# Kernel tuning notes

Measured on AMD Instinct MI355X. Metric: run time of the kernel, lower is better.

## Reference

```python
import jax, jax.numpy as jnp
import numpy as np
from jax import lax

POOL = 2  # pool_kernel

def _conv2d(x, w, b, stride=1):
    # x: [N,C,H,W], w: [O,I,kh,kw] (torch OIHW layout)
    y = lax.conv_general_dilated(
        x, w, window_strides=(stride, stride), padding='VALID',
        dimension_numbers=('NCHW', 'OIHW', 'NCHW'))
    return y + b[None, :, None, None]

def _maxpool(x, k):
    return lax.reduce_window(x, -jnp.inf, lax.max,
                             (1, 1, k, k), (1, 1, k, k), 'VALID')

def setup_inputs() -> dict:
    key = jax.random.key(0)
    ks = jax.random.split(key, 8)
    B, S, D = 8, 64, 128
    C = 32  # num_channels, depth=3 -> channels 1->32->64->64
    def kaiming(k, shape):
        fan_in = shape[1] * shape[2] * shape[3]
        return jax.random.normal(k, shape, jnp.float32) * np.float32(np.sqrt(2.0 / fan_in))
    return {
        'token_features': jax.random.normal(ks[0], (B, S, D), jnp.float32),
        'type_embedds': jax.random.normal(ks[1], (B, S, D), jnp.float32),
        'w0': kaiming(ks[2], (C, 1, 3, 3)),
        'b0': jnp.zeros((C,), jnp.float32),
        'w1': kaiming(ks[3], (2 * C, C, 3, 3)),
        'b1': jnp.zeros((2 * C,), jnp.float32),
        'w2': kaiming(ks[4], (2 * C, 2 * C, 3, 3)),
        'b2': jnp.zeros((2 * C,), jnp.float32),
    }

def reference(token_features, type_embedds, w0, b0, w1, b1, w2, b2):
    B, S, D = type_embedds.shape
    # Outter2dFusion: ger(gate, features) -> fused[b,s,i,j] = type[b,s,i]*token[b,s,j]
    fused = jnp.einsum('bsi,bsj->bsij', type_embedds, token_features)
    x = fused.reshape(B * S, 1, D, D)  # each token's d x d map as 1-channel image
    gelu = lambda t: jax.nn.gelu(t, approximate=False)  # torch GELU default (erf)
    x = _maxpool(gelu(_conv2d(x, w0, b0, stride=1)), POOL)
    x = _maxpool(gelu(_conv2d(x, w1, b1, stride=1)), POOL)
    x = _maxpool(gelu(_conv2d(x, w2, b2, stride=1)), POOL)
    # dropout is identity at inference
    return x.reshape(B, S, -1)
```

## Files before the change

### kernel.cpp

```cpp
#include <hip/hip_runtime.h>


typedef short short8 __attribute__((ext_vector_type(8)));
typedef _Float16 half8 __attribute__((ext_vector_type(8)));
typedef float f32x4 __attribute__((ext_vector_type(4)));
typedef unsigned int uint4v __attribute__((ext_vector_type(4)));

#define OFF_TY   0
#define OFF_H16  544
#define OFF_P0   32800
#define OFF_P1   100384
#define OFF_TK   OFF_P0
#define LDS_TOTAL 123936

__device__ __forceinline__ unsigned short f2bf(float f) {
    unsigned int u = __float_as_uint(f);
    u += 0x7fffu + ((u >> 16) & 1u);
    return (unsigned short)(u >> 16);
}

__device__ __forceinline__ unsigned int pack2h(float a, float b) {
    union { _Float16 h[2]; unsigned int u; } p;
    p.h[0] = (_Float16)a;
    p.h[1] = (_Float16)b;
    return p.u;
}

__device__ __forceinline__ float gelu_f(float x) {
    float ax = __builtin_fabsf(x);
    float E  = __builtin_amdgcn_exp2f(x * x * -0.72134752f);
    float k  = __builtin_amdgcn_rcpf(__builtin_fmaf(0.33267686f, ax, 1.0f));
    float s  = __builtin_fmaf(0.7478556f, k, -0.0958798f);
    s = __builtin_fmaf(s, k, 0.3480242f);
    s = s * k;
    float erfabs = __builtin_fmaf(-s, E, 1.0f);
    return __builtin_fmaf(0.5f * ax, erfabs, 0.5f * x);
}

__device__ __forceinline__ void conv0_burst(char* smem, const float* tys,
                                            int w, int l15, int lc,
                                            float b00, float b01, int pbase) {
    const int y_base = 2 * pbase;
    half8 afrag;
    {
        float a0 = tys[y_base + l15 + 0];
        float a1 = tys[y_base + l15 + 1];
        float a2 = tys[y_base + l15 + 2];
        float a3 = tys[y_base + l15 + 3];
        union { uint4v u; half8 h; } av;
        av.u = (uint4v){ pack2h(a0, a1), pack2h(a2, a3), 0u, 0u };
        afrag = av.h;
    }
    const f32x4 ci0 = (f32x4){b00, b00, b00, b00};
    const f32x4 ci1 = (f32x4){b01, b01, b01, b01};
    const int base = (w < 4) ? w * 12 : 48 + (w - 4) * 20;
    const int cnt  = (w < 4) ? 12 : ((w == 7) ? 18 : 20);

    #pragma unroll
    for (int j = 0; j < 20; ++j) {
        if (j < cnt) {
            const int uid = base + j;
            const int q  = uid >> 1;
            const int ct = uid & 1;
            const char* hp = smem + OFF_H16 + ((2*q)*32 + ct*16 + l15) * 8;
            uint2 hA = *(const uint2*)(hp);
            uint2 hB = *(const uint2*)(hp + 256);
            if (lc != 0) { hA.x = 0u; hA.y = 0u; hB.x = 0u; hB.y = 0u; }
            union { uint4v u; half8 h; } ba, bb;
            ba.u = (uint4v){hA.x, hA.y, 0u, 0u};
            bb.u = (uint4v){hB.x, hB.y, 0u, 0u};
            const f32x4 ci = ct ? ci1 : ci0;
            f32x4 cA = __builtin_amdgcn_mfma_f32_16x16x32_f16(afrag, ba.h, ci, 0, 0, 0);
            f32x4 cB = __builtin_amdgcn_mfma_f32_16x16x32_f16(afrag, bb.h, ci, 0, 0, 0);
            float m0 = gelu_f(fmaxf(fmaxf(cA[0], cA[1]), fmaxf(cB[0], cB[1])));
            float m1 = gelu_f(fmaxf(fmaxf(cA[2], cA[3]), fmaxf(cB[2], cB[3])));
            const int c = ct * 16 + l15;
            const int upos = (q >> 1) * 8 + ((4 * (q & 1) + (c >> 3)) ^ ((q >> 1) & 7));
            const int p0 = pbase + 2 * lc;
            const int s0 = p0 & 15, s1 = (p0 + 1) & 15;
            *(unsigned short*)(smem + OFF_P0 + (s0 * 264 + upos) * 16 + (c & 7) * 2) = f2bf(m0);
            *(unsigned short*)(smem + OFF_P0 + (s1 * 264 + upos) * 16 + (c & 7) * 2) = f2bf(m1);
        }
    }
}

__launch_bounds__(512, 2)
__global__ void conv_pipeline(const float* __restrict__ token,
                              const float* __restrict__ type_,
                              const float* __restrict__ w0, const float* __restrict__ b0,
                              const float* __restrict__ w1, const float* __restrict__ b1,
                              const float* __restrict__ w2, const float* __restrict__ b2,
                              float* __restrict__ out) {
    extern __shared__ char smem[];
    float* tys = (float*)(smem + OFF_TY);
    float* tks = (float*)(smem + OFF_TK);

    const int tid = threadIdx.x;
    const int img = blockIdx.x;
    const int w   = tid >> 6;
    const int l   = tid & 63;
    const int l15 = l & 15;
    const int lc  = l >> 4;
    const int c0w = tid & 31;

    for (int i = tid; i < 132; i += 512) {
        tys[i] = (i < 128) ? type_[img*128 + i] : 0.f;
        if (i < 128) tks[i] = token[img*128 + i];
    }

    const float b00 = b0[l15];
    const float b01 = b0[l15 + 16];

    __syncthreads();

    {
        float w0r[9];
        #pragma unroll
        for (int i = 0; i < 9; ++i) w0r[i] = w0[c0w*9 + i];
        int x = tid >> 5;
        #pragma unroll
        for (int k = 0; k < 8; ++k, x += 16) {
            if (x < 126) {
                float t0 = tks[x], t1 = tks[x+1], t2 = tks[x+2];
                float h0 = __builtin_fmaf(w0r[0],t0, __builtin_fmaf(w0r[1],t1, w0r[2]*t2));
                float h1 = __builtin_fmaf(w0r[3],t0, __builtin_fmaf(w0r[4],t1, w0r[5]*t2));
                float h2 = __builtin_fmaf(w0r[6],t0, __builtin_fmaf(w0r[7],t1, w0r[8]*t2));
                uint2 hv; hv.x = pack2h(h0, h1); hv.y = pack2h(h2, 0.f);
                *(uint2*)(smem + OFF_H16 + (x*32 + c0w)*8) = hv;
            }
        }
    }

    short8 wf[18];
    float bias;
    const int ch = ((w & 3) * 16) + l15;
    if (w < 4) {
        bias = b1[ch];
        #pragma unroll
        for (int uv = 0; uv < 9; ++uv) {
            short8 f;
            #pragma unroll
            for (int j = 0; j < 8; ++j)
                f[j] = (short)f2bf(w1[(ch*32 + 8*lc + j)*9 + uv]);
            wf[uv] = f;
        }
    } else {
        bias = b2[ch];
        #pragma unroll
        for (int kh = 0; kh < 2; ++kh)
            #pragma unroll
            for (int uv = 0; uv < 9; ++uv) {
                short8 f;
                #pragma unroll
                for (int j = 0; j < 8; ++j)
                    f[j] = (short)f2bf(w2[(ch*64 + kh*32 + 8*lc + j)*9 + uv]);
                wf[kh*9 + uv] = f;
            }
    }

    __syncthreads();

    conv0_burst(smem, tys, w, l15, lc, b00, b01, 0);
    __syncthreads();

    const size_t obase = (size_t)img * 12544;

    for (int i1 = 0; i1 < 30; ++i1) {
        if (w < 4) {
            int rbase = (i1 % 6) * 30;
            int xr = ch >> 3;
            #pragma unroll
            for (int half = 0; half < 2; ++half) {
                f32x4 acc[4];
                #pragma unroll
                for (int i = 0; i < 4; ++i) acc[i] = (f32x4){0.f,0.f,0.f,0.f};
                #pragma unroll
                for (int pr = 0; pr < 4; ++pr) {
                    int sbase = ((2*i1 + pr) & 15) * 264;
                    #pragma unroll
                    for (int v = 0; v < 3; ++v) {
                        #pragma unroll
                        for (int mtl = 0; mtl < 2; ++mtl) {
                            int col = (2*half + mtl)*16 + l15 + v;
                            int unit = sbase + (col>>1)*8 + ((4*(col&1) + lc) ^ ((col>>1)&7));
                            short8 a = *(const short8*)(smem + OFF_P0 + unit*16);
                            if (pr <= 2)
                                acc[mtl*2+0] = __builtin_amdgcn_mfma_f32_16x16x32_bf16(
                                    a, wf[pr*3+v], acc[mtl*2+0], 0, 0, 0);
                            if (pr >= 1)
                                acc[mtl*2+1] = __builtin_amdgcn_mfma_f32_16x16x32_bf16(
                                    a, wf[(pr-1)*3+v], acc[mtl*2+1], 0, 0, 0);
                        }
                    }
                }
                #pragma unroll
                for (int mtl = 0; mtl < 2; ++mtl) {
                    int pcol = (2*half + mtl)*8 + lc*2;
                    if (pcol < 30) {
                        f32x4 A0 = acc[mtl*2+0], A1 = acc[mtl*2+1];
                        float p0 = fmaxf(fmaxf(A0[0], A0[1]), fmaxf(A1[0], A1[1]));
                        float p1 = fmaxf(fmaxf(A0[2], A0[3]), fmaxf(A1[2], A1[3]));
                        float m0 = gelu_f(p0 + bias);
                        float m1 = gelu_f(p1 + bias);
                        int u0 = (rbase + pcol)*8     + (xr ^ (pcol & 7));
                        int u1 = (rbase + pcol + 1)*8 + (xr ^ ((pcol+1) & 7));
                        *(unsigned short*)(smem + OFF_P1 + u0*16 + (ch&7)*2) = f2bf(m0);
                        *(unsigned short*)(smem + OFF_P1 + u1*16 + (ch&7)*2) = f2bf(m1);
                    }
                }
            }
        } else if (i1 >= 4 && (i1 & 1) == 0) {
            const int i2 = (i1 - 4) >> 1;
            f32x4 acc[4];
            #pragma unroll
            for (int i = 0; i < 4; ++i) acc[i] = (f32x4){0.f,0.f,0.f,0.f};
            #pragma unroll
            for (int pr = 0; pr < 4; ++pr) {
                int rb = ((2*i2 + pr) % 6) * 30;
                #pragma unroll
                for (int v = 0; v < 3; ++v) {
                    #pragma unroll
                    for (int mt = 0; mt < 2; ++mt) {
                        int col = mt*16 + l15 + v;
                        #pragma unroll
                        for (int kh = 0; kh < 2; ++kh) {
                            int unit = (rb + col)*8 + ((kh*4 + lc) ^ (col & 7));
                            short8 a = *(const short8*)(smem + OFF_P1 + unit*16);
                            if (pr <= 2)
                                acc[mt*2+0] = __builtin_amdgcn_mfma_f32_16x16x32_bf16(
                                    a, wf[kh*9 + pr*3+v], acc[mt*2+0], 0, 0, 0);
                            if (pr >= 1)
                                acc[mt*2+1] = __builtin_amdgcn_mfma_f32_16x16x32_bf16(
                                    a, wf[kh*9 + (pr-1)*3+v], acc[mt*2+1], 0, 0, 0);
                        }
                    }
                }
            }
            #pragma unroll
            for (int mt = 0; mt < 2; ++mt) {
                int pcol = mt*8 + lc*2;
                if (pcol < 14) {
                    f32x4 A0 = acc[mt*2+0], A1 = acc[mt*2+1];
                    float g00 = gelu_f(A0[0] + bias), g01 = gelu_f(A0[1] + bias);
                    float g02 = gelu_f(A0[2] + bias), g03 = gelu_f(A0[3] + bias);
                    float g10 = gelu_f(A1[0] + bias), g11 = gelu_f(A1[1] + bias);
                    float g12 = gelu_f(A1[2] + bias), g13 = gelu_f(A1[3] + bias);
                    float m0 = fmaxf(fmaxf(g00, g01), fmaxf(g10, g11));
                    float m1 = fmaxf(fmaxf(g02, g03), fmaxf(g12, g13));
                    float2 st; st.x = m0; st.y = m1;
                    *(float2*)(out + obase + ch*196 + i2*14 + pcol) = st;
                }
            }
        }

        if ((i1 & 3) == 2) conv0_burst(smem, tys, w, l15, lc, b00, b01, 2*i1 + 4);

        __syncthreads();
    }

    if (w >= 4) {
        const int i2 = 13;
        f32x4 acc[4];
        #pragma unroll
        for (int i = 0; i < 4; ++i) acc[i] = (f32x4){0.f,0.f,0.f,0.f};
        #pragma unroll
        for (int pr = 0; pr < 4; ++pr) {
            int rb = ((2*i2 + pr) % 6) * 30;
            #pragma unroll
            for (int v = 0; v < 3; ++v) {
                #pragma unroll
                for (int mt = 0; mt < 2; ++mt) {
                    int col = mt*16 + l15 + v;
                    #pragma unroll
                    for (int kh = 0; kh < 2; ++kh) {
                        int unit = (rb + col)*8 + ((kh*4 + lc) ^ (col & 7));
                        short8 a = *(const short8*)(smem + OFF_P1 + unit*16);
                        if (pr <= 2)
                            acc[mt*2+0] = __builtin_amdgcn_mfma_f32_16x16x32_bf16(
                                a, wf[kh*9 + pr*3+v], acc[mt*2+0], 0, 0, 0);
                        if (pr >= 1)
                            acc[mt*2+1] = __builtin_amdgcn_mfma_f32_16x16x32_bf16(
                                a, wf[kh*9 + (pr-1)*3+v], acc[mt*2+1], 0, 0, 0);
                    }
                }
            }
        }
        #pragma unroll
        for (int mt = 0; mt < 2; ++mt) {
            int pcol = mt*8 + lc*2;
            if (pcol < 14) {
                f32x4 A0 = acc[mt*2+0], A1 = acc[mt*2+1];
                float g00 = gelu_f(A0[0] + bias), g01 = gelu_f(A0[1] + bias);
                float g02 = gelu_f(A0[2] + bias), g03 = gelu_f(A0[3] + bias);
                float g10 = gelu_f(A1[0] + bias), g11 = gelu_f(A1[1] + bias);
                float g12 = gelu_f(A1[2] + bias), g13 = gelu_f(A1[3] + bias);
                float m0 = fmaxf(fmaxf(g00, g01), fmaxf(g10, g11));
                float m1 = fmaxf(fmaxf(g02, g03), fmaxf(g12, g13));
                float2 st; st.x = m0; st.y = m1;
                *(float2*)(out + obase + ch*196 + i2*14 + pcol) = st;
            }
        }
    }
}

extern "C" void kernel_launch(void* const* d_in, const int* in_sizes, int n_in,
                              void* d_out, int out_size, void* d_ws, size_t ws_size,
                              hipStream_t stream) {
    const float* token = (const float*)d_in[0];
    const float* type_ = (const float*)d_in[1];
    const float* w0 = (const float*)d_in[2];
    const float* b0 = (const float*)d_in[3];
    const float* w1 = (const float*)d_in[4];
    const float* b1 = (const float*)d_in[5];
    const float* w2 = (const float*)d_in[6];
    const float* b2 = (const float*)d_in[7];
    float* out = (float*)d_out;

    hipLaunchKernelGGL(conv_pipeline, dim3(512), dim3(512), LDS_TOTAL, stream,
                       token, type_, w0, b0, w1, b1, w2, b2, out);
}
```

Measured before the change: 187.3 us.

## Double block size to 1024 threads and split conv work across 16 waves

Raises the workgroup from 8 to 16 waves. Conv1 waves each take one half of the columns instead of looping over both halves, conv2 waves each take one M-tile, and the conv0 burst units are redistributed across 16 waves. This gives more waves per image to hide MFMA and LDS latency, at the cost of a lower occupancy bound (one block per CU) and tighter register limits under the 1024-thread launch bound.

After: 251.4 us. +34.2%, slower.

```diff
diff --git a/kernel.cpp b/kernel.cpp
--- a/kernel.cpp
+++ b/kernel.cpp
@@ -53,11 +53,11 @@
     }
     const f32x4 ci0 = (f32x4){b00, b00, b00, b00};
     const f32x4 ci1 = (f32x4){b01, b01, b01, b01};
-    const int base = (w < 4) ? w * 12 : 48 + (w - 4) * 20;
-    const int cnt  = (w < 4) ? 12 : ((w == 7) ? 18 : 20);
+    const int base = (w < 8) ? w * 6 : 48 + (w - 8) * 10;
+    const int cnt  = (w < 8) ? 6 : ((w == 15) ? 8 : 10);
 
     #pragma unroll
-    for (int j = 0; j < 20; ++j) {
+    for (int j = 0; j < 10; ++j) {
         if (j < cnt) {
             const int uid = base + j;
             const int q  = uid >> 1;
@@ -84,7 +84,7 @@
     }
 }
 
-__launch_bounds__(512, 2)
+__launch_bounds__(1024, 1)
 __global__ void conv_pipeline(const float* __restrict__ token,
                               const float* __restrict__ type_,
                               const float* __restrict__ w0, const float* __restrict__ b0,
@@ -103,7 +103,7 @@
     const int lc  = l >> 4;
     const int c0w = tid & 31;
 
-    for (int i = tid; i < 132; i += 512) {
+    for (int i = tid; i < 132; i += 1024) {
         tys[i] = (i < 128) ? type_[img*128 + i] : 0.f;
         if (i < 128) tks[i] = token[img*128 + i];
     }
@@ -119,7 +119,7 @@
         for (int i = 0; i < 9; ++i) w0r[i] = w0[c0w*9 + i];
         int x = tid >> 5;
         #pragma unroll
-        for (int k = 0; k < 8; ++k, x += 16) {
+        for (int k = 0; k < 4; ++k, x += 32) {
             if (x < 126) {
                 float t0 = tks[x], t1 = tks[x+1], t2 = tks[x+2];
                 float h0 = __builtin_fmaf(w0r[0],t0, __builtin_fmaf(w0r[1],t1, w0r[2]*t2));
@@ -134,7 +134,7 @@
     short8 wf[18];
     float bias;
     const int ch = ((w & 3) * 16) + l15;
-    if (w < 4) {
+    if (w < 8) {
         bias = b1[ch];
         #pragma unroll
         for (int uv = 0; uv < 9; ++uv) {
@@ -166,139 +166,123 @@
     const size_t obase = (size_t)img * 12544;
 
     for (int i1 = 0; i1 < 30; ++i1) {
-        if (w < 4) {
+        if (w < 8) {
+            const int half = w >> 2;
             int rbase = (i1 % 6) * 30;
             int xr = ch >> 3;
-            #pragma unroll
-            for (int half = 0; half < 2; ++half) {
-                f32x4 acc[4];
+            f32x4 acc[4];
+            #pragma unroll
+            for (int i = 0; i < 4; ++i) acc[i] = (f32x4){0.f,0.f,0.f,0.f};
+            #pragma unroll
+            for (int pr = 0; pr < 4; ++pr) {
+                int sbase = ((2*i1 + pr) & 15) * 264;
                 #pragma unroll
-                for (int i = 0; i < 4; ++i) acc[i] = (f32x4){0.f,0.f,0.f,0.f};
-                #pragma unroll
-                for (int pr = 0; pr < 4; ++pr) {
-                    int sbase = ((2*i1 + pr) & 15) * 264;
+                for (int v = 0; v < 3; ++v) {
                     #pragma unroll
-                    for (int v = 0; v < 3; ++v) {
-                        #pragma unroll
-                        for (int mtl = 0; mtl < 2; ++mtl) {
-                            int col = (2*half + mtl)*16 + l15 + v;
-                            int unit = sbase + (col>>1)*8 + ((4*(col&1) + lc) ^ ((col>>1)&7));
-                            short8 a = *(const short8*)(smem + OFF_P0 + unit*16);
-                            if (pr <= 2)
-                                acc[mtl*2+0] = __builtin_amdgcn_mfma_f32_16x16x32_bf16(
-                                    a, wf[pr*3+v], acc[mtl*2+0], 0, 0, 0);
-                            if (pr >= 1)
-                                acc[mtl*2+1] = __builtin_amdgcn_mfma_f32_16x16x32_bf16(
-                                    a, wf[(pr-1)*3+v], acc[mtl*2+1], 0, 0, 0);
-                        }
+                    for (int mtl = 0; mtl < 2; ++mtl) {
+                        int col = (2*half + mtl)*16 + l15 + v;
+                        int unit = sbase + (col>>1)*8 + ((4*(col&1) + lc) ^ ((col>>1)&7));
+                        short8 a = *(const short8*)(smem + OFF_P0 + unit*16);
+                        if (pr <= 2)
+                            acc[mtl*2+0] = __builtin_amdgcn_mfma_f32_16x16x32_bf16(
+                                a, wf[pr*3+v], acc[mtl*2+0], 0, 0, 0);
+                        if (pr >= 1)
+                            acc[mtl*2+1] = __builtin_amdgcn_mfma_f32_16x16x32_bf16(
+                                a, wf[(pr-1)*3+v], acc[mtl*2+1], 0, 0, 0);
                     }
                 }
-                #pragma unroll
-                for (int mtl = 0; mtl < 2; ++mtl) {
-                    int pcol = (2*half + mtl)*8 + lc*2;
-                    if (pcol < 30) {
-                        f32x4 A0 = acc[mtl*2+0], A1 = acc[mtl*2+1];
-                        float p0 = fmaxf(fmaxf(A0[0], A0[1]), fmaxf(A1[0], A1[1]));
-                        float p1 = fmaxf(fmaxf(A0[2], A0[3]), fmaxf(A1[2], A1[3]));
-                        float m0 = gelu_f(p0 + bias);
-                        float m1 = gelu_f(p1 + bias);
-                        int u0 = (rbase + pcol)*8     + (xr ^ (pcol & 7));
-                        int u1 = (rbase + pcol + 1)*8 + (xr ^ ((pcol+1) & 7));
-                        *(unsigned short*)(smem + OFF_P1 + u0*16 + (ch&7)*2) = f2bf(m0);
-                        *(unsigned short*)(smem + OFF_P1 + u1*16 + (ch&7)*2) = f2bf(m1);
-                    }
+            }
+            #pragma unroll
+            for (int mtl = 0; mtl < 2; ++mtl) {
+                int pcol = (2*half + mtl)*8 + lc*2;
+                if (pcol < 30) {
+                    f32x4 A0 = acc[mtl*2+0], A1 = acc[mtl*2+1];
+                    float p0 = fmaxf(fmaxf(A0[0], A0[1]), fmaxf(A1[0], A1[1]));
+                    float p1 = fmaxf(fmaxf(A0[2], A0[3]), fmaxf(A1[2], A1[3]));
+                    float m0 = gelu_f(p0 + bias);
+                    float m1 = gelu_f(p1 + bias);
+                    int u0 = (rbase + pcol)*8     + (xr ^ (pcol & 7));
+                    int u1 = (rbase + pcol + 1)*8 + (xr ^ ((pcol+1) & 7));
+                    *(unsigned short*)(smem + OFF_P1 + u0*16 + (ch&7)*2) = f2bf(m0);
+                    *(unsigned short*)(smem + OFF_P1 + u1*16 + (ch&7)*2) = f2bf(m1);
                 }
             }
         } else if (i1 >= 4 && (i1 & 1) == 0) {
             const int i2 = (i1 - 4) >> 1;
-            f32x4 acc[4];
-            #pragma unroll
-            for (int i = 0; i < 4; ++i) acc[i] = (f32x4){0.f,0.f,0.f,0.f};
+            const int mt = (w >> 2) & 1;
+            f32x4 acc0 = (f32x4){0.f,0.f,0.f,0.f};
+            f32x4 acc1 = (f32x4){0.f,0.f,0.f,0.f};
             #pragma unroll
             for (int pr = 0; pr < 4; ++pr) {
                 int rb = ((2*i2 + pr) % 6) * 30;
                 #pragma unroll
                 for (int v = 0; v < 3; ++v) {
-                    #pragma unroll
-                    for (int mt = 0; mt < 2; ++mt) {
-                        int col = mt*16 + l15 + v;
-                        #pragma unroll
-                        for (int kh = 0; kh < 2; ++kh) {
-                            int unit = (rb + col)*8 + ((kh*4 + lc) ^ (col & 7));
-                            short8 a = *(const short8*)(smem + OFF_P1 + unit*16);
-                            if (pr <= 2)
-                                acc[mt*2+0] = __builtin_amdgcn_mfma_f32_16x16x32_bf16(
-                                    a, wf[kh*9 + pr*3+v], acc[mt*2+0], 0, 0, 0);
-                            if (pr >= 1)
-                                acc[mt*2+1] = __builtin_amdgcn_mfma_f32_16x16x32_bf16(
-                                    a, wf[kh*9 + (pr-1)*3+v], acc[mt*2+1], 0, 0, 0);
-                        }
-                    }
-                }
-            }
-            #pragma unroll
-            for (int mt = 0; mt < 2; ++mt) {
-                int pcol = mt*8 + lc*2;
-                if (pcol < 14) {
-                    f32x4 A0 = acc[mt*2+0], A1 = acc[mt*2+1];
-                    float g00 = gelu_f(A0[0] + bias), g01 = gelu_f(A0[1] + bias);
-                    float g02 = gelu_f(A0[2] + bias), g03 = gelu_f(A0[3] + bias);
-                    float g10 = gelu_f(A1[0] + bias), g11 = gelu_f(A1[1] + bias);
-                    float g12 = gelu_f(A1[2] + bias), g13 = gelu_f(A1[3] + bias);
-                    float m0 = fmaxf(fmaxf(g00, g01), fmaxf(g10, g11));
-                    float m1 = fmaxf(fmaxf(g02, g03), fmaxf(g12, g13));
-                    float2 st; st.x = m0; st.y = m1;
-                    *(float2*)(out + obase + ch*196 + i2*14 + pcol) = st;
-                }
-            }
-        }
-
-        if ((i1 & 3) == 2) conv0_burst(smem, tys, w, l15, lc, b00, b01, 2*i1 + 4);
-
-        __syncthreads();
-    }
-
-    if (w >= 4) {
-        const int i2 = 13;
-        f32x4 acc[4];
-        #pragma unroll
-        for (int i = 0; i < 4; ++i) acc[i] = (f32x4){0.f,0.f,0.f,0.f};
-        #pragma unroll
-        for (int pr = 0; pr < 4; ++pr) {
-            int rb = ((2*i2 + pr) % 6) * 30;
-            #pragma unroll
-            for (int v = 0; v < 3; ++v) {
-                #pragma unroll
-                for (int mt = 0; mt < 2; ++mt) {
                     int col = mt*16 + l15 + v;
                     #pragma unroll
                     for (int kh = 0; kh < 2; ++kh) {
                         int unit = (rb + col)*8 + ((kh*4 + lc) ^ (col & 7));
                         short8 a = *(const short8*)(smem + OFF_P1 + unit*16);
                         if (pr <= 2)
-                            acc[mt*2+0] = __builtin_amdgcn_mfma_f32_16x16x32_bf16(
-                                a, wf[kh*9 + pr*3+v], acc[mt*2+0], 0, 0, 0);
+                            acc0 = __builtin_amdgcn_mfma_f32_16x16x32_bf16(
+                                a, wf[kh*9 + pr*3+v], acc0, 0, 0, 0);
                         if (pr >= 1)
-                            acc[mt*2+1] = __builtin_amdgcn_mfma_f32_16x16x32_bf16(
-                                a, wf[kh*9 + (pr-1)*3+v], acc[mt*2+1], 0, 0, 0);
+                            acc1 = __builtin_amdgcn_mfma_f32_16x16x32_bf16(
+                                a, wf[kh*9 + (pr-1)*3+v], acc1, 0, 0, 0);
                     }
                 }
             }
-        }
-        #pragma unroll
-        for (int mt = 0; mt < 2; ++mt) {
             int pcol = mt*8 + lc*2;
             if (pcol < 14) {
-                f32x4 A0 = acc[mt*2+0], A1 = acc[mt*2+1];
-                float g00 = gelu_f(A0[0] + bias), g01 = gelu_f(A0[1] + bias);
-                float g02 = gelu_f(A0[2] + bias), g03 = gelu_f(A0[3] + bias);
-                float g10 = gelu_f(A1[0] + bias), g11 = gelu_f(A1[1] + bias);
-                float g12 = gelu_f(A1[2] + bias), g13 = gelu_f(A1[3] + bias);
+                float g00 = gelu_f(acc0[0] + bias), g01 = gelu_f(acc0[1] + bias);
+                float g02 = gelu_f(acc0[2] + bias), g03 = gelu_f(acc0[3] + bias);
+                float g10 = gelu_f(acc1[0] + bias), g11 = gelu_f(acc1[1] + bias);
+                float g12 = gelu_f(acc1[2] + bias), g13 = gelu_f(acc1[3] + bias);
                 float m0 = fmaxf(fmaxf(g00, g01), fmaxf(g10, g11));
                 float m1 = fmaxf(fmaxf(g02, g03), fmaxf(g12, g13));
                 float2 st; st.x = m0; st.y = m1;
                 *(float2*)(out + obase + ch*196 + i2*14 + pcol) = st;
             }
+        }
+
+        if ((i1 & 3) == 2) conv0_burst(smem, tys, w, l15, lc, b00, b01, 2*i1 + 4);
+
+        __syncthreads();
+    }
+
+    if (w >= 8) {
+        const int i2 = 13;
+        const int mt = (w >> 2) & 1;
+        f32x4 acc0 = (f32x4){0.f,0.f,0.f,0.f};
+        f32x4 acc1 = (f32x4){0.f,0.f,0.f,0.f};
+        #pragma unroll
+        for (int pr = 0; pr < 4; ++pr) {
+            int rb = ((2*i2 + pr) % 6) * 30;
+            #pragma unroll
+            for (int v = 0; v < 3; ++v) {
+                int col = mt*16 + l15 + v;
+                #pragma unroll
+                for (int kh = 0; kh < 2; ++kh) {
+                    int unit = (rb + col)*8 + ((kh*4 + lc) ^ (col & 7));
+                    short8 a = *(const short8*)(smem + OFF_P1 + unit*16);
+                    if (pr <= 2)
+                        acc0 = __builtin_amdgcn_mfma_f32_16x16x32_bf16(
+                            a, wf[kh*9 + pr*3+v], acc0, 0, 0, 0);
+                    if (pr >= 1)
+                        acc1 = __builtin_amdgcn_mfma_f32_16x16x32_bf16(
+                            a, wf[kh*9 + (pr-1)*3+v], acc1, 0, 0, 0);
+                }
+            }
+        }
+        int pcol = mt*8 + lc*2;
+        if (pcol < 14) {
+            float g00 = gelu_f(acc0[0] + bias), g01 = gelu_f(acc0[1] + bias);
+            float g02 = gelu_f(acc0[2] + bias), g03 = gelu_f(acc0[3] + bias);
+            float g10 = gelu_f(acc1[0] + bias), g11 = gelu_f(acc1[1] + bias);
+            float g12 = gelu_f(acc1[2] + bias), g13 = gelu_f(acc1[3] + bias);
+            float m0 = fmaxf(fmaxf(g00, g01), fmaxf(g10, g11));
+            float m1 = fmaxf(fmaxf(g02, g03), fmaxf(g12, g13));
+            float2 st; st.x = m0; st.y = m1;
+            *(float2*)(out + obase + ch*196 + i2*14 + pcol) = st;
         }
     }
 }
@@ -316,6 +300,6 @@
     const float* b2 = (const float*)d_in[7];
     float* out = (float*)d_out;
 
-    hipLaunchKernelGGL(conv_pipeline, dim3(512), dim3(512), LDS_TOTAL, stream,
+    hipLaunchKernelGGL(conv_pipeline, dim3(512), dim3(1024), LDS_TOTAL, stream,
                        token, type_, w0, b0, w1, b1, w2, b2, out);
 }
```

## Split conv2 over two iterations, halve barriers, and raise MFMA wave priority

Applied to the files above, without the earlier changes.

Splits each conv2 output row's accumulation across two consecutive loop iterations, keeping the accumulators live in registers between them. This balances conv2 work against conv1 work every iteration instead of every other one. It also moves the conv0 burst earlier, issues __syncthreads only on odd iterations, and wraps the MFMA sections in s_setprio. The aim is to cut idle time for the conv2 waves and barrier overhead, at the cost of more register pressure and tighter ring-buffer hazard margins.

Result: slower. 462.9 us, median of 2 (+147.1%).

```diff
diff --git a/kernel.cpp b/kernel.cpp
--- a/kernel.cpp
+++ b/kernel.cpp
@@ -165,10 +165,13 @@
 
     const size_t obase = (size_t)img * 12544;
 
+    f32x4 c2acc[4];
+
     for (int i1 = 0; i1 < 30; ++i1) {
         if (w < 4) {
             int rbase = (i1 % 6) * 30;
             int xr = ch >> 3;
+            __builtin_amdgcn_s_setprio(1);
             #pragma unroll
             for (int half = 0; half < 2; ++half) {
                 f32x4 acc[4];
@@ -193,6 +196,7 @@
                         }
                     }
                 }
+                __builtin_amdgcn_s_setprio(0);
                 #pragma unroll
                 for (int mtl = 0; mtl < 2; ++mtl) {
                     int pcol = (2*half + mtl)*8 + lc*2;
@@ -208,14 +212,19 @@
                         *(unsigned short*)(smem + OFF_P1 + u1*16 + (ch&7)*2) = f2bf(m1);
                     }
                 }
-            }
-        } else if (i1 >= 4 && (i1 & 1) == 0) {
+                if (half == 0) __builtin_amdgcn_s_setprio(1);
+            }
+        } else if (i1 >= 4) {
             const int i2 = (i1 - 4) >> 1;
-            f32x4 acc[4];
-            #pragma unroll
-            for (int i = 0; i < 4; ++i) acc[i] = (f32x4){0.f,0.f,0.f,0.f};
-            #pragma unroll
-            for (int pr = 0; pr < 4; ++pr) {
+            const int prlo = (i1 & 1) ? 2 : 0;
+            if ((i1 & 1) == 0) {
+                #pragma unroll
+                for (int i = 0; i < 4; ++i) c2acc[i] = (f32x4){0.f,0.f,0.f,0.f};
+            }
+            __builtin_amdgcn_s_setprio(1);
+            #pragma unroll
+            for (int prr = 0; prr < 2; ++prr) {
+                const int pr = prlo + prr;
                 int rb = ((2*i2 + pr) % 6) * 30;
                 #pragma unroll
                 for (int v = 0; v < 3; ++v) {
@@ -227,35 +236,39 @@
                             int unit = (rb + col)*8 + ((kh*4 + lc) ^ (col & 7));
                             short8 a = *(const short8*)(smem + OFF_P1 + unit*16);
                             if (pr <= 2)
-                                acc[mt*2+0] = __builtin_amdgcn_mfma_f32_16x16x32_bf16(
-                                    a, wf[kh*9 + pr*3+v], acc[mt*2+0], 0, 0, 0);
+                                c2acc[mt*2+0] = __builtin_amdgcn_mfma_f32_16x16x32_bf16(
+                                    a, wf[kh*9 + pr*3+v], c2acc[mt*2+0], 0, 0, 0);
                             if (pr >= 1)
-                                acc[mt*2+1] = __builtin_amdgcn_mfma_f32_16x16x32_bf16(
-                                    a, wf[kh*9 + (pr-1)*3+v], acc[mt*2+1], 0, 0, 0);
+                                c2acc[mt*2+1] = __builtin_amdgcn_mfma_f32_16x16x32_bf16(
+                                    a, wf[kh*9 + (pr-1)*3+v], c2acc[mt*2+1], 0, 0, 0);
                         }
                     }
                 }
             }
-            #pragma unroll
-            for (int mt = 0; mt < 2; ++mt) {
-                int pcol = mt*8 + lc*2;
-                if (pcol < 14) {
-                    f32x4 A0 = acc[mt*2+0], A1 = acc[mt*2+1];
-                    float g00 = gelu_f(A0[0] + bias), g01 = gelu_f(A0[1] + bias);
-                    float g02 = gelu_f(A0[2] + bias), g03 = gelu_f(A0[3] + bias);
-                    float g10 = gelu_f(A1[0] + bias), g11 = gelu_f(A1[1] + bias);
-                    float g12 = gelu_f(A1[2] + bias), g13 = gelu_f(A1[3] + bias);
-                    float m0 = fmaxf(fmaxf(g00, g01), fmaxf(g10, g11));
-                    float m1 = fmaxf(fmaxf(g02, g03), fmaxf(g12, g13));
-                    float2 st; st.x = m0; st.y = m1;
-                    *(float2*)(out + obase + ch*196 + i2*14 + pcol) = st;
-                }
-            }
-        }
-
-        if ((i1 & 3) == 2) conv0_burst(smem, tys, w, l15, lc, b00, b01, 2*i1 + 4);
-
-        __syncthreads();
+            __builtin_amdgcn_s_setprio(0);
+            if (i1 & 1) {
+                #pragma unroll
+                for (int mt = 0; mt < 2; ++mt) {
+                    int pcol = mt*8 + lc*2;
+                    if (pcol < 14) {
+                        f32x4 A0 = c2acc[mt*2+0], A1 = c2acc[mt*2+1];
+                        float g00 = gelu_f(A0[0] + bias), g01 = gelu_f(A0[1] + bias);
+                        float g02 = gelu_f(A0[2] + bias), g03 = gelu_f(A0[3] + bias);
+                        float g10 = gelu_f(A1[0] + bias), g11 = gelu_f(A1[1] + bias);
+                        float g12 = gelu_f(A1[2] + bias), g13 = gelu_f(A1[3] + bias);
+                        float m0 = fmaxf(fmaxf(g00, g01), fmaxf(g10, g11));
+                        float m1 = fmaxf(fmaxf(g02, g03), fmaxf(g12, g13));
+                        float2 st; st.x = m0; st.y = m1;
+                        *(float2*)(out + obase + ch*196 + i2*14 + pcol) = st;
+                    }
+                }
+            }
+        }
+
+        if ((i1 & 3) == 1 && i1 <= 25)
+            conv0_burst(smem, tys, w, l15, lc, b00, b01, 2*i1 + 6);
+
+        if (i1 & 1) __syncthreads();
     }
 
     if (w >= 4) {
```
